# Kernel tuning notes

Hardware: AMD Instinct MI355X
Metric: run time of the kernel (lower is better)

Reference implementation:

```python
import jax, jax.numpy as jnp
import numpy as np

EPS = 1e-3  # keras BatchNormalization default epsilon

def _spatial_shift(x):
    # x: [B, T, N, C]; channel c is circularly rolled along N by (c % N)
    B, T, N, C = x.shape
    shifts = np.arange(C) % N                      # [C]
    pos = np.arange(N)[:, None]                    # [N,1]
    # tf.roll(shift=s) moves element j to (j+s) % N, i.e. out[j] = in[(j - s) % N]
    gather_idx = (pos - shifts[None, :]) % N       # [N, C]
    return x[:, :, gather_idx, np.arange(C)]       # advanced indexing -> [B,T,N,C]

def setup_inputs() -> dict:
    key = jax.random.key(0)
    k1, k2, k3 = jax.random.split(key, 3)
    B, T, N, C_in, F = 8, 64, 21, 128, 256
    x = jax.random.normal(k1, (B, T, N, C_in), dtype=jnp.float32)
    W = jax.random.normal(k2, (C_in, F), dtype=jnp.float32) * (1.0 / np.sqrt(C_in))
    b = jnp.zeros((F,), dtype=jnp.float32)
    gamma = jnp.ones((F,), dtype=jnp.float32)
    beta = jnp.zeros((F,), dtype=jnp.float32)
    return {"x": x, "W": W, "b": b, "gamma": gamma, "beta": beta}

def reference(x, W, b, gamma, beta):
    # per-channel circular shift along N
    xs = _spatial_shift(x)                               # [B,T,N,C]
    # 1x1 conv == matmul over channel dim
    y = jnp.einsum('btnc,cf->btnf', xs, W) + b           # [B,T,N,F]
    # BatchNormalization with training=True: batch statistics over B,T,N
    mean = jnp.mean(y, axis=(0, 1, 2))
    var = jnp.var(y, axis=(0, 1, 2))
    y = (y - mean) * jax.lax.rsqrt(var + EPS) * gamma + beta
    return jax.nn.relu(y)
```

## Files before the change

### kernel.cpp

```cpp
#include <hip/hip_runtime.h>


#define NPOS 21
#define CIN  128
#define FOUT 256
#define BT   512
#define M_TOTAL 10752
#define BN_EPS 1e-3f
#define LROW 24
#define CK   16

template<int R0, int NV, bool F4F>
__device__ __forceinline__ void conv_rg(const float* __restrict__ xsS,
                                        const float* __restrict__ W,
                                        const float* __restrict__ bias,
                                        float* __restrict__ yout,
                                        float* __restrict__ sumL,
                                        float* __restrict__ sqL,
                                        int fb, int rg)
{
    float acc[6][4];
    #pragma unroll
    for (int jr = 0; jr < 6; jr++)
        acc[jr][0] = acc[jr][1] = acc[jr][2] = acc[jr][3] = 0.0f;

    #pragma unroll
    for (int ck = 0; ck < CIN / CK; ck++) {
        float4 w[CK];
        #pragma unroll
        for (int j = 0; j < CK; j++)
            w[j] = *(const float4*)(W + (size_t)(ck * CK + j) * FOUT + fb);

        #pragma unroll
        for (int j = 0; j < CK; j++) {
            const float* xc = xsS + (ck * CK + j) * LROW;
            float xv[6];
            if (F4F) {
                float4 a = *(const float4*)(xc + R0);
                float2 b = *(const float2*)(xc + R0 + 4);
                xv[0] = a.x; xv[1] = a.y; xv[2] = a.z; xv[3] = a.w;
                xv[4] = b.x; xv[5] = b.y;
            } else {
                float2 b = *(const float2*)(xc + R0);
                float4 a = *(const float4*)(xc + R0 + 2);
                xv[0] = b.x; xv[1] = b.y;
                xv[2] = a.x; xv[3] = a.y; xv[4] = a.z; xv[5] = a.w;
            }
            #pragma unroll
            for (int jr = 0; jr < 6; jr++) {
                acc[jr][0] = fmaf(xv[jr], w[j].x, acc[jr][0]);
                acc[jr][1] = fmaf(xv[jr], w[j].y, acc[jr][1]);
                acc[jr][2] = fmaf(xv[jr], w[j].z, acc[jr][2]);
                acc[jr][3] = fmaf(xv[jr], w[j].w, acc[jr][3]);
            }
        }
    }

    const float4 bv = *(const float4*)(bias + fb);
    float ls0 = 0.f, ls1 = 0.f, ls2 = 0.f, ls3 = 0.f;
    float lq0 = 0.f, lq1 = 0.f, lq2 = 0.f, lq3 = 0.f;
    #pragma unroll
    for (int jr = 0; jr < NV; jr++) {
        float4 o;
        o.x = acc[jr][0] + bv.x;
        o.y = acc[jr][1] + bv.y;
        o.z = acc[jr][2] + bv.z;
        o.w = acc[jr][3] + bv.w;
        *(float4*)(yout + (size_t)(R0 + jr) * FOUT + fb) = o;
        ls0 += o.x; lq0 += o.x * o.x;
        ls1 += o.y; lq1 += o.y * o.y;
        ls2 += o.z; lq2 += o.z * o.z;
        ls3 += o.w; lq3 += o.w * o.w;
    }
    *(float4*)(sumL + rg * FOUT + fb) = make_float4(ls0, ls1, ls2, ls3);
    *(float4*)(sqL  + rg * FOUT + fb) = make_float4(lq0, lq1, lq2, lq3);
}

__global__ __launch_bounds__(256) void k_conv(const float* __restrict__ x,
                                              const float* __restrict__ W,
                                              const float* __restrict__ bias,
                                              float* __restrict__ y,
                                              float* __restrict__ ws)
{
    __shared__ float xsS[CIN * LROW];
    __shared__ float sumL[4 * FOUT];
    __shared__ float sqL [4 * FOUT];

    const int bt = blockIdx.x;
    const int t  = threadIdx.x;

    const float* xin = x + (size_t)bt * (NPOS * CIN);
    for (int i = t; i < NPOS * CIN; i += 256) {
        float v = xin[i];
        int r = i >> 7;
        int c = i & (CIN - 1);
        int s = c % NPOS;
        int n = r + s; if (n >= NPOS) n -= NPOS;
        xsS[c * LROW + n] = v;
    }
    if (t < CIN) {
        xsS[t * LROW + 21] = 0.0f;
        xsS[t * LROW + 22] = 0.0f;
        xsS[t * LROW + 23] = 0.0f;
    }
    __syncthreads();

    const int rg = t >> 6;
    const int fb = (t & 63) << 2;
    float* yout = y + (size_t)bt * (NPOS * FOUT);

    if      (rg == 0) conv_rg< 0, 6, true >(xsS, W, bias, yout, sumL, sqL, fb, rg);
    else if (rg == 1) conv_rg< 6, 6, false>(xsS, W, bias, yout, sumL, sqL, fb, rg);
    else if (rg == 2) conv_rg<12, 6, true >(xsS, W, bias, yout, sumL, sqL, fb, rg);
    else              conv_rg<18, 3, false>(xsS, W, bias, yout, sumL, sqL, fb, rg);
    __syncthreads();

    float s = sumL[t] + sumL[FOUT + t] + sumL[2 * FOUT + t] + sumL[3 * FOUT + t];
    float q = sqL[t]  + sqL[FOUT + t]  + sqL[2 * FOUT + t]  + sqL[3 * FOUT + t];
    atomicAdd(ws + t, s);
    atomicAdd(ws + FOUT + t, q);
}

__global__ void k_zero(float* __restrict__ ws)
{
    ws[blockIdx.x * 256 + threadIdx.x] = 0.0f;
}

#define BN_BLOCKS 1344

__global__ __launch_bounds__(256) void k_bnapply(float* __restrict__ y,
                                                 const float* __restrict__ ws,
                                                 const float* __restrict__ gamma,
                                                 const float* __restrict__ beta)
{
    const int t  = threadIdx.x;
    const int fb = (t & 63) << 2;
    const float4 sm = *(const float4*)(ws + fb);
    const float4 sq = *(const float4*)(ws + FOUT + fb);
    const float4 gm = *(const float4*)(gamma + fb);
    const float4 be = *(const float4*)(beta + fb);
    const float invM = 1.0f / (float)M_TOTAL;

    float sc[4], bs[4];
    {
        float m0 = sm.x * invM, m1 = sm.y * invM, m2 = sm.z * invM, m3 = sm.w * invM;
        float v0 = fmaf(-m0, m0, sq.x * invM);
        float v1 = fmaf(-m1, m1, sq.y * invM);
        float v2 = fmaf(-m2, m2, sq.z * invM);
        float v3 = fmaf(-m3, m3, sq.w * invM);
        sc[0] = rsqrtf(v0 + BN_EPS) * gm.x;  bs[0] = be.x - m0 * sc[0];
        sc[1] = rsqrtf(v1 + BN_EPS) * gm.y;  bs[1] = be.y - m1 * sc[1];
        sc[2] = rsqrtf(v2 + BN_EPS) * gm.z;  bs[2] = be.z - m2 * sc[2];
        sc[3] = rsqrtf(v3 + BN_EPS) * gm.w;  bs[3] = be.w - m3 * sc[3];
    }

    float4* y4 = (float4*)y;
    #pragma unroll
    for (int it = 0; it < 2; it++) {
        int g = blockIdx.x * 512 + it * 256 + t;
        float4 v = y4[g];
        v.x = fmaxf(fmaf(v.x, sc[0], bs[0]), 0.0f);
        v.y = fmaxf(fmaf(v.y, sc[1], bs[1]), 0.0f);
        v.z = fmaxf(fmaf(v.z, sc[2], bs[2]), 0.0f);
        v.w = fmaxf(fmaf(v.w, sc[3], bs[3]), 0.0f);
        y4[g] = v;
    }
}

extern "C" __global__ void SpatialShiftConvBlock_71923522339050_kernel() {}

extern "C" void kernel_launch(void* const* d_in, const int* in_sizes, int n_in,
                              void* d_out, int out_size, void* d_ws, size_t ws_size,
                              hipStream_t stream) {
    float* y  = (float*)d_out;
    float* ws = (float*)d_ws;
    k_zero<<<2, 256, 0, stream>>>(ws);
    k_conv<<<BT, 256, 0, stream>>>((const float*)d_in[0], (const float*)d_in[1],
                                   (const float*)d_in[2], y, ws);
    k_bnapply<<<BN_BLOCKS, 256, 0, stream>>>(y, ws,
                                             (const float*)d_in[3], (const float*)d_in[4]);
}
```

Before: 96.53 us.

## Split conv output channels across two blocks per (b,t) to double grid size

Each (b,t) slice is now handled by two blocks, each computing half of the 256 output channels with two channels per thread instead of four. This doubles the grid from 512 to 1024 blocks and halves per-thread accumulators, aiming for better CU occupancy and latency hiding on a 256-CU device. The cost is that each block redoes the shifted input load into shared memory, and per-thread arithmetic intensity drops because each x value is reused across fewer weights.

Measured after the change: 99.17 us. 2.7% more time.

```diff
diff --git a/kernel.cpp b/kernel.cpp
--- a/kernel.cpp
+++ b/kernel.cpp
@@ -12,24 +12,23 @@
 
 template<int R0, int NV, bool F4F>
 __device__ __forceinline__ void conv_rg(const float* __restrict__ xsS,
-                                        const float* __restrict__ W,
-                                        const float* __restrict__ bias,
-                                        float* __restrict__ yout,
+                                        const float* __restrict__ Wc,
+                                        const float* __restrict__ biasc,
+                                        float* __restrict__ youtc,
                                         float* __restrict__ sumL,
                                         float* __restrict__ sqL,
-                                        int fb, int rg)
+                                        int lc, int rg)
 {
-    float acc[6][4];
+    float acc[6][2];
     #pragma unroll
-    for (int jr = 0; jr < 6; jr++)
-        acc[jr][0] = acc[jr][1] = acc[jr][2] = acc[jr][3] = 0.0f;
+    for (int jr = 0; jr < 6; jr++) { acc[jr][0] = 0.0f; acc[jr][1] = 0.0f; }
 
     #pragma unroll
     for (int ck = 0; ck < CIN / CK; ck++) {
-        float4 w[CK];
+        float2 w[CK];
         #pragma unroll
         for (int j = 0; j < CK; j++)
-            w[j] = *(const float4*)(W + (size_t)(ck * CK + j) * FOUT + fb);
+            w[j] = *(const float2*)(Wc + (size_t)(ck * CK + j) * FOUT);
 
         #pragma unroll
         for (int j = 0; j < CK; j++) {
@@ -50,30 +49,23 @@
             for (int jr = 0; jr < 6; jr++) {
                 acc[jr][0] = fmaf(xv[jr], w[j].x, acc[jr][0]);
                 acc[jr][1] = fmaf(xv[jr], w[j].y, acc[jr][1]);
-                acc[jr][2] = fmaf(xv[jr], w[j].z, acc[jr][2]);
-                acc[jr][3] = fmaf(xv[jr], w[j].w, acc[jr][3]);
             }
         }
     }
 
-    const float4 bv = *(const float4*)(bias + fb);
-    float ls0 = 0.f, ls1 = 0.f, ls2 = 0.f, ls3 = 0.f;
-    float lq0 = 0.f, lq1 = 0.f, lq2 = 0.f, lq3 = 0.f;
+    const float2 bv = *(const float2*)biasc;
+    float ls0 = 0.f, ls1 = 0.f, lq0 = 0.f, lq1 = 0.f;
     #pragma unroll
     for (int jr = 0; jr < NV; jr++) {
-        float4 o;
+        float2 o;
         o.x = acc[jr][0] + bv.x;
         o.y = acc[jr][1] + bv.y;
-        o.z = acc[jr][2] + bv.z;
-        o.w = acc[jr][3] + bv.w;
-        *(float4*)(yout + (size_t)(R0 + jr) * FOUT + fb) = o;
+        *(float2*)(youtc + (size_t)(R0 + jr) * FOUT) = o;
         ls0 += o.x; lq0 += o.x * o.x;
         ls1 += o.y; lq1 += o.y * o.y;
-        ls2 += o.z; lq2 += o.z * o.z;
-        ls3 += o.w; lq3 += o.w * o.w;
     }
-    *(float4*)(sumL + rg * FOUT + fb) = make_float4(ls0, ls1, ls2, ls3);
-    *(float4*)(sqL  + rg * FOUT + fb) = make_float4(lq0, lq1, lq2, lq3);
+    *(float2*)(sumL + rg * 128 + lc) = make_float2(ls0, ls1);
+    *(float2*)(sqL  + rg * 128 + lc) = make_float2(lq0, lq1);
 }
 
 __global__ __launch_bounds__(256) void k_conv(const float* __restrict__ x,
@@ -83,10 +75,11 @@
                                               float* __restrict__ ws)
 {
     __shared__ float xsS[CIN * LROW];
-    __shared__ float sumL[4 * FOUT];
-    __shared__ float sqL [4 * FOUT];
+    __shared__ float sumL[4 * 128];
+    __shared__ float sqL [4 * 128];
 
-    const int bt = blockIdx.x;
+    const int bt = blockIdx.x >> 1;
+    const int bh = blockIdx.x & 1;
     const int t  = threadIdx.x;
 
     const float* xin = x + (size_t)bt * (NPOS * CIN);
@@ -106,19 +99,26 @@
     __syncthreads();
 
     const int rg = t >> 6;
-    const int fb = (t & 63) << 2;
-    float* yout = y + (size_t)bt * (NPOS * FOUT);
+    const int lc = (t & 63) << 1;
+    const int ch = bh * 128 + lc;
+    const float* Wc    = W + ch;
+    const float* biasc = bias + ch;
+    float* youtc = y + (size_t)bt * (NPOS * FOUT) + ch;
 
-    if      (rg == 0) conv_rg< 0, 6, true >(xsS, W, bias, yout, sumL, sqL, fb, rg);
-    else if (rg == 1) conv_rg< 6, 6, false>(xsS, W, bias, yout, sumL, sqL, fb, rg);
-    else if (rg == 2) conv_rg<12, 6, true >(xsS, W, bias, yout, sumL, sqL, fb, rg);
-    else              conv_rg<18, 3, false>(xsS, W, bias, yout, sumL, sqL, fb, rg);
+    if      (rg == 0) conv_rg< 0, 6, true >(xsS, Wc, biasc, youtc, sumL, sqL, lc, rg);
+    else if (rg == 1) conv_rg< 6, 6, false>(xsS, Wc, biasc, youtc, sumL, sqL, lc, rg);
+    else if (rg == 2) conv_rg<12, 6, true >(xsS, Wc, biasc, youtc, sumL, sqL, lc, rg);
+    else              conv_rg<18, 3, false>(xsS, Wc, biasc, youtc, sumL, sqL, lc, rg);
     __syncthreads();
 
-    float s = sumL[t] + sumL[FOUT + t] + sumL[2 * FOUT + t] + sumL[3 * FOUT + t];
-    float q = sqL[t]  + sqL[FOUT + t]  + sqL[2 * FOUT + t]  + sqL[3 * FOUT + t];
-    atomicAdd(ws + t, s);
-    atomicAdd(ws + FOUT + t, q);
+    if (t < 128) {
+        float s = sumL[t] + sumL[128 + t] + sumL[256 + t] + sumL[384 + t];
+        atomicAdd(ws + bh * 128 + t, s);
+    } else {
+        int u = t - 128;
+        float q = sqL[u] + sqL[128 + u] + sqL[256 + u] + sqL[384 + u];
+        atomicAdd(ws + FOUT + bh * 128 + u, q);
+    }
 }
 
 __global__ void k_zero(float* __restrict__ ws)
@@ -175,8 +175,8 @@
     float* y  = (float*)d_out;
     float* ws = (float*)d_ws;
     k_zero<<<2, 256, 0, stream>>>(ws);
-    k_conv<<<BT, 256, 0, stream>>>((const float*)d_in[0], (const float*)d_in[1],
-                                   (const float*)d_in[2], y, ws);
+    k_conv<<<2 * BT, 256, 0, stream>>>((const float*)d_in[0], (const float*)d_in[1],
+                                       (const float*)d_in[2], y, ws);
     k_bnapply<<<BN_BLOCKS, 256, 0, stream>>>(y, ws,
                                              (const float*)d_in[3], (const float*)d_in[4]);
 }
```
